# Performance work log

Hardware: AMD Instinct MI355X
Metric: run time of the kernel (lower is better)

## Reference

```python
import jax, jax.numpy as jnp
import numpy as np

N_DIM = 1024   # nodes (rows of s, rows of Kweight)
IN_DIM = 1024  # nodes / feature dim (cols of s, rows of Qweight, side of Gmat)
H_DIM = 64
B = 16


def setup_inputs() -> dict:
    key = jax.random.key(0)
    k1, k2, k3, k4 = jax.random.split(key, 4)
    s = jax.random.normal(k1, (N_DIM, B, IN_DIM), dtype=jnp.float32)
    Gmat = jax.random.uniform(k2, (IN_DIM, IN_DIM), dtype=jnp.float32)
    # torch init: rand * (4/d)**0.5 - (1/d)**0.5  => U[-(1/d)**0.5, (1/d)**0.5]... kept faithful
    Qweight = jax.random.uniform(k3, (IN_DIM, H_DIM), dtype=jnp.float32) * (4.0 / IN_DIM) ** 0.5 - (1.0 / IN_DIM) ** 0.5
    Kweight = jax.random.uniform(k4, (N_DIM, H_DIM), dtype=jnp.float32) * (4.0 / N_DIM) ** 0.5 - (1.0 / N_DIM) ** 0.5
    return {"s": s, "Gmat": Gmat, "Qweight": Qweight, "Kweight": Kweight}


def reference(s, Gmat, Qweight, Kweight):
    h_dim = Qweight.shape[1]
    inv_sqrt_h = 1.0 / jnp.sqrt(jnp.float32(h_dim))
    # q: einsum('ijk,km->ijm', s, Qw).permute(1,0,2) -> (B, n, h)
    q = jnp.einsum('nbi,ih->bnh', s, Qweight)
    # k: s.permute(1,2,0) einsum Kw then permute(0,2,1) -> (B, h, i)
    k = jnp.einsum('nbi,nh->bhi', s, Kweight)
    # squared (non-softmax) attention scores: (B, n, i)
    att = jnp.square(jnp.einsum('bnh,bhi->bni', q, k) * inv_sqrt_h + 1e-9)
    # adjacency aggregation: (B, n, i) @ (i, i)
    att = jnp.einsum('bni,ij->bnj', att, Gmat)
    # row-normalize and permute back to (n, B, i)
    s_t = jnp.sum(att, axis=2, keepdims=True) + 0.001
    return (att / s_t).transpose(1, 0, 2)
```

## Files before the change

### kernel.cpp

```cpp
#include <hip/hip_runtime.h>
#include <hip/hip_bf16.h>
#include <stdint.h>

typedef unsigned short u16;
typedef unsigned int   u32;

#define N_DIM  1024
#define IN_DIM 1024
#define H_DIM  64
#define BATCH  16

typedef __bf16 bf16x8 __attribute__((ext_vector_type(8)));
typedef float  f32x4  __attribute__((ext_vector_type(4)));

__device__ inline u16 f2bf(float f) {
    union { float f; u32 u; } v; v.f = f;
    u32 u = v.u;
    return (u16)((u + 0x7fffu + ((u >> 16) & 1u)) >> 16);
}
__device__ inline u32 pack2(float a, float b) {
    __hip_bfloat162 h = __float22bfloat162_rn(float2{a, b});
    union { __hip_bfloat162 h; u32 u; } cv; cv.h = h; return cv.u;
}

__device__ inline void gl_lds16(const u16* g, u16* l) {
    __builtin_amdgcn_global_load_lds(
        (const __attribute__((address_space(1))) u32*)g,
        (__attribute__((address_space(3))) u32*)l, 16, 0, 0);
}

__global__ void prep_w(const float* __restrict__ Q, const float* __restrict__ Kw,
                       u16* __restrict__ QT, u16* __restrict__ KwT) {
    int idx = blockIdx.x * 256 + threadIdx.x;
    const float* src = (idx < 65536) ? Q : Kw;
    u16* dst = (idx < 65536) ? QT : KwT;
    int i = idx & 65535;
    int h = i >> 10;
    int n = i & 1023;
    dst[h * 1024 + n] = f2bf(src[n * 64 + h]);
}

__global__ void prep_g(const float* __restrict__ G, u16* __restrict__ Gbt,
                       float* __restrict__ Grsum) {
    __shared__ float tile[64][65];
    int i0 = blockIdx.y * 64, j0 = blockIdx.x * 64;
    int tx = threadIdx.x & 63, ty = threadIdx.x >> 6;
    for (int r = 0; r < 16; ++r) {
        int i = ty * 16 + r;
        tile[i][tx] = G[(size_t)(i0 + i) * 1024 + j0 + tx];
    }
    __syncthreads();
    for (int r = 0; r < 16; ++r) {
        int j = ty * 16 + r;
        Gbt[(size_t)(j0 + j) * 1024 + i0 + tx] = f2bf(tile[tx][j]);
    }
    if (ty == 0) {
        float sum = 0.f;
        for (int j = 0; j < 64; ++j) sum += tile[tx][j];
        atomicAdd(&Grsum[i0 + tx], sum);
    }
}

__global__ __launch_bounds__(512) void gemm_q(
        const float* __restrict__ s, const u16* __restrict__ QT,
        u16* __restrict__ qws) {
    int b = blockIdx.y;
    int n0 = blockIdx.x * 64;
    __shared__ __align__(16) float red[4096];
    int t = threadIdx.x, lane = t & 63, w = t >> 6, quad = lane >> 4, l15 = lane & 15;
    int wm = (w & 3) * 16;
    int kb = (w >> 2) * 512;
    const float* arow = s + (size_t)(n0 + wm + l15) * (BATCH * IN_DIM)
                          + (size_t)b * IN_DIM + kb + quad * 8;
    const u16* bbase = QT + (size_t)l15 * 1024 + kb + quad * 8;

    f32x4 acc[4] = {};
    float4 A0[2], A1[2];
    bf16x8 Bf[2][4];
    A0[0] = ((const float4*)arow)[0];
    A1[0] = ((const float4*)arow)[1];
#pragma unroll
    for (int ct = 0; ct < 4; ++ct)
        Bf[0][ct] = *(const bf16x8*)&bbase[ct * 16384];

#pragma unroll
    for (int st = 0; st < 16; ++st) {
        int cur = st & 1, nxt = cur ^ 1;
        if (st < 15) {
            const float4* ap = (const float4*)(arow + (size_t)(st + 1) * 32);
            A0[nxt] = ap[0];
            A1[nxt] = ap[1];
#pragma unroll
            for (int ct = 0; ct < 4; ++ct)
                Bf[nxt][ct] = *(const bf16x8*)&bbase[ct * 16384 + (st + 1) * 32];
        }
        float4 fa = A0[cur], fb = A1[cur];
        union { uint4 u; bf16x8 v; } cu;
        cu.u = (uint4){ pack2(fa.x, fa.y), pack2(fa.z, fa.w),
                        pack2(fb.x, fb.y), pack2(fb.z, fb.w) };
#pragma unroll
        for (int ct = 0; ct < 4; ++ct)
            acc[ct] = __builtin_amdgcn_mfma_f32_16x16x32_bf16(cu.v, Bf[cur][ct], acc[ct], 0, 0, 0);
    }

    if (w >= 4) {
        float* dst = red + ((w - 4) * 64 + lane) * 16;
#pragma unroll
        for (int ct = 0; ct < 4; ++ct) *(f32x4*)&dst[ct * 4] = acc[ct];
    }
    __syncthreads();
    if (w < 4) {
        const float* sp2 = red + (w * 64 + lane) * 16;
        u16* ob = qws + (size_t)b * 65536;
#pragma unroll
        for (int ct = 0; ct < 4; ++ct) {
            f32x4 o = *(const f32x4*)&sp2[ct * 4];
#pragma unroll
            for (int r = 0; r < 4; ++r) {
                int m = n0 + wm + quad * 4 + r;
                ob[(size_t)m * 64 + ct * 16 + l15] = f2bf(acc[ct][r] + o[r]);
            }
        }
    }
}

__global__ __launch_bounds__(512) void gemm_kt(
        const float* __restrict__ s, const u16* __restrict__ KwT,
        u16* __restrict__ ktws) {
    int b = blockIdx.y;
    int i0 = blockIdx.x * 64;
    __shared__ __align__(16) u16 As[2][2][64][34];
    int t = threadIdx.x, lane = t & 63, w = t >> 6, quad = lane >> 4, l15 = lane & 15;
    int half = w >> 2;
    int wm = (w & 3) * 16;
    int shalf = t >> 8, nr = (t & 255) >> 3, iofs = (t & 7) * 8;
    const float* sp = s + (size_t)(shalf * 512 + nr) * (BATCH * IN_DIM)
                        + (size_t)b * IN_DIM + i0 + iofs;
    const u16* bbase = KwT + (size_t)l15 * 1024 + half * 512 + quad * 8;

    f32x4 acc[4] = {};
    float4 P0[2], P1[2];
    bf16x8 Bf[2][4];
    P0[0] = ((const float4*)sp)[0];
    P1[0] = ((const float4*)sp)[1];
    {
        const float4* p = (const float4*)(sp + (size_t)32 * 16384);
        P0[1] = p[0]; P1[1] = p[1];
    }
#pragma unroll
    for (int ct = 0; ct < 4; ++ct)
        Bf[0][ct] = *(const bf16x8*)&bbase[ct * 16384];

#pragma unroll
    for (int c = 0; c < 16; ++c) {
        int buf = c & 1;
        float4 fa = P0[buf], fb = P1[buf];
        u16* wp = &As[shalf][buf][iofs][nr];
        wp[0]   = f2bf(fa.x);
        wp[34]  = f2bf(fa.y);
        wp[68]  = f2bf(fa.z);
        wp[102] = f2bf(fa.w);
        wp[136] = f2bf(fb.x);
        wp[170] = f2bf(fb.y);
        wp[204] = f2bf(fb.z);
        wp[238] = f2bf(fb.w);
        __syncthreads();
        if (c < 14) {
            const float4* p = (const float4*)(sp + (size_t)(c + 2) * 32 * 16384);
            P0[buf] = p[0]; P1[buf] = p[1];
        }
        if (c < 15) {
#pragma unroll
            for (int ct = 0; ct < 4; ++ct)
                Bf[(c + 1) & 1][ct] = *(const bf16x8*)&bbase[ct * 16384 + (c + 1) * 32];
        }
        const u32* ap = (const u32*)&As[half][buf][wm + l15][quad * 8];
        union { u32 u[4]; bf16x8 v; } au;
        au.u[0] = ap[0]; au.u[1] = ap[1]; au.u[2] = ap[2]; au.u[3] = ap[3];
#pragma unroll
        for (int ct = 0; ct < 4; ++ct)
            acc[ct] = __builtin_amdgcn_mfma_f32_16x16x32_bf16(au.v, Bf[buf][ct], acc[ct], 0, 0, 0);
    }

    __syncthreads();
    float* red = (float*)As;
    if (w >= 4) {
        float* dst = red + ((w - 4) * 64 + lane) * 16;
#pragma unroll
        for (int ct = 0; ct < 4; ++ct) *(f32x4*)&dst[ct * 4] = acc[ct];
    }
    __syncthreads();
    if (w < 4) {
        const float* sp2 = red + (w * 64 + lane) * 16;
        u16* ob = ktws + (size_t)b * 65536;
#pragma unroll
        for (int ct = 0; ct < 4; ++ct) {
            f32x4 o = *(const f32x4*)&sp2[ct * 4];
#pragma unroll
            for (int r = 0; r < 4; ++r) {
                int i = i0 + wm + quad * 4 + r;
                ob[(size_t)i * 64 + ct * 16 + l15] = f2bf(acc[ct][r] + o[r]);
            }
        }
    }
}

__global__ __launch_bounds__(256, 2) void gemm_fused(
        const u16* __restrict__ qws, const u16* __restrict__ ktws,
        const u16* __restrict__ Gbt, const float* __restrict__ Grsum,
        float* __restrict__ out) {
    int b = blockIdx.z;
    int n0 = blockIdx.x * 256, m0 = blockIdx.y * 128;
    const u16* qb = qws  + (size_t)b * 65536;
    const u16* kb = ktws + (size_t)b * 65536;
    __shared__ __align__(16) u16 As[128 * 40];
    __shared__ __align__(16) u16 Bs[2][256 * 32];
    __shared__ __align__(16) u16 ktc[32 * 72];
    __shared__ __align__(16) float Grs[1024];
    __shared__ float rs[128];
    int t = threadIdx.x, lane = t & 63, w = t >> 6, quad = lane >> 4, l15 = lane & 15;
    int ti = w & 1;
    int wm = (w >> 1) * 64;
    int wn = (w & 1) * 128;

    ((float4*)Grs)[t] = ((const float4*)Grsum)[t];
    if (t < 128) rs[t] = 0.f;

    bf16x8 qf[4][2];
    for (int j = 0; j < 4; ++j)
        for (int kick = 0; kick < 2; ++kick)
            qf[j][kick] = *(const bf16x8*)&qb[(size_t)(m0 + wm + j*16 + l15) * 64 + kick*32 + quad*8];

    int br = t >> 2, bc = (t & 3) * 8;
    for (int g4 = 0; g4 < 4; ++g4)
        gl_lds16(Gbt + (size_t)(n0 + br + g4*64) * 1024 + bc, &Bs[0][(br + g4*64) * 32 + bc]);
    int ir = t >> 3, ch = (t & 7) * 8;
    uint4 kreg = *(const uint4*)&kb[(size_t)ir * 64 + ch];

    f32x4 acc[4][8] = {};
    float partial[4] = {0.f, 0.f, 0.f, 0.f};

    for (int kk = 0; kk < 32; ++kk) {
        int buf = kk & 1;
        *(uint4*)&ktc[ir * 72 + ch] = kreg;
        __syncthreads();
        f32x4 sacc[4] = {};
        for (int kick = 0; kick < 2; ++kick) {
            bf16x8 ktf = *(const bf16x8*)&ktc[(ti*16 + l15) * 72 + kick*32 + quad*8];
            for (int j = 0; j < 4; ++j)
                sacc[j] = __builtin_amdgcn_mfma_f32_16x16x32_bf16(ktf, qf[j][kick], sacc[j], 0, 0, 0);
        }
        if (kk < 31)
            kreg = *(const uint4*)&kb[(size_t)((kk + 1) * 32 + ir) * 64 + ch];
        float4 g = *(const float4*)&Grs[kk * 32 + ti * 16 + quad * 4];
        for (int j = 0; j < 4; ++j) {
            float v0 = sacc[j][0] * 0.125f + 1e-9f; v0 *= v0;
            float v1 = sacc[j][1] * 0.125f + 1e-9f; v1 *= v1;
            float v2 = sacc[j][2] * 0.125f + 1e-9f; v2 *= v2;
            float v3 = sacc[j][3] * 0.125f + 1e-9f; v3 *= v3;
            partial[j] += v0 * g.x + v1 * g.y + v2 * g.z + v3 * g.w;
            uint2 pk = { pack2(v0, v1), pack2(v2, v3) };
            *(uint2*)&As[(wm + j*16 + l15) * 40 + ti*16 + quad*4] = pk;
        }
        __syncthreads();
        if (kk < 31) {
            for (int g4 = 0; g4 < 4; ++g4)
                gl_lds16(Gbt + (size_t)(n0 + br + g4*64) * 1024 + (kk+1)*32 + bc,
                         &Bs[buf^1][(br + g4*64) * 32 + bc]);
        }
        int kh = quad * 8;
        bf16x8 af[4];
        for (int i = 0; i < 4; ++i) af[i] = *(const bf16x8*)&As[(wm + i*16 + l15) * 40 + kh];
        for (int jh = 0; jh < 2; ++jh) {
            bf16x8 bfr[4];
            for (int j = 0; j < 4; ++j)
                bfr[j] = *(const bf16x8*)&Bs[buf][(wn + jh*64 + j*16 + l15) * 32 + kh];
            for (int i = 0; i < 4; ++i)
                for (int j = 0; j < 4; ++j)
                    acc[i][jh*4 + j] = __builtin_amdgcn_mfma_f32_16x16x32_bf16(af[i], bfr[j], acc[i][jh*4 + j], 0, 0, 0);
        }
    }

    for (int j = 0; j < 4; ++j) {
        partial[j] += __shfl_xor(partial[j], 16, 64);
        partial[j] += __shfl_xor(partial[j], 32, 64);
    }
    if (quad == 0)
        for (int j = 0; j < 4; ++j) atomicAdd(&rs[wm + j*16 + l15], partial[j]);
    __syncthreads();
    if (t < 128) rs[t] = 1.0f / (rs[t] + 0.001f);
    __syncthreads();

    for (int i = 0; i < 4; ++i) {
        float4 rv = *(const float4*)&rs[wm + i * 16 + quad * 4];
        float rva[4] = { rv.x, rv.y, rv.z, rv.w };
        for (int r = 0; r < 4; ++r) {
            int m = m0 + wm + i * 16 + quad * 4 + r;
            float* orow = out + (size_t)m * (BATCH * IN_DIM) + (size_t)b * IN_DIM + n0 + wn;
            for (int j = 0; j < 8; ++j)
                orow[j * 16 + l15] = acc[i][j][r] * rva[r];
        }
    }
}

extern "C" void kernel_launch(void* const* d_in, const int* in_sizes, int n_in,
                              void* d_out, int out_size, void* d_ws, size_t ws_size,
                              hipStream_t stream) {
    const float* s  = (const float*)d_in[0];
    const float* G  = (const float*)d_in[1];
    const float* Q  = (const float*)d_in[2];
    const float* Kw = (const float*)d_in[3];
    float* out = (float*)d_out;
    char* ws = (char*)d_ws;

    u16*   qws   = (u16*)(ws + (size_t)(32u << 20));
    u16*   ktws  = qws + (size_t)16 * 65536;
    u16*   Gbt   = (u16*)(ws + (size_t)(36u << 20));
    u16*   QT    = (u16*)(ws + (size_t)(38u << 20));
    u16*   KwT   = (u16*)(ws + (size_t)(38u << 20) + (128u << 10));
    float* Grsum = (float*)(ws + (size_t)(38u << 20) + (256u << 10));

    hipMemsetAsync(Grsum, 0, 1024 * sizeof(float), stream);
    prep_w<<<512, 256, 0, stream>>>(Q, Kw, QT, KwT);
    prep_g<<<dim3(16, 16), 256, 0, stream>>>(G, Gbt, Grsum);
    gemm_q<<<dim3(16, 16), 512, 0, stream>>>(s, QT, qws);
    gemm_kt<<<dim3(16, 16), 512, 0, stream>>>(s, KwT, ktws);
    gemm_fused<<<dim3(4, 8, 16), 256, 0, stream>>>(qws, ktws, Gbt, Grsum, out);
}
```

Baseline: 204.9 us.

## Merge prep and projection kernels, swizzle G tile LDS, deepen q prefetch

```diff
diff --git a/kernel.cpp b/kernel.cpp
--- a/kernel.cpp
+++ b/kernel.cpp
@@ -29,21 +29,24 @@
         (__attribute__((address_space(3))) u32*)l, 16, 0, 0);
 }
 
-__global__ void prep_w(const float* __restrict__ Q, const float* __restrict__ Kw,
-                       u16* __restrict__ QT, u16* __restrict__ KwT) {
-    int idx = blockIdx.x * 256 + threadIdx.x;
-    const float* src = (idx < 65536) ? Q : Kw;
-    u16* dst = (idx < 65536) ? QT : KwT;
-    int i = idx & 65535;
-    int h = i >> 10;
-    int n = i & 1023;
-    dst[h * 1024 + n] = f2bf(src[n * 64 + h]);
-}
-
-__global__ void prep_g(const float* __restrict__ G, u16* __restrict__ Gbt,
-                       float* __restrict__ Grsum) {
+__global__ __launch_bounds__(256) void prep(
+        const float* __restrict__ G, const float* __restrict__ Q,
+        const float* __restrict__ Kw, u16* __restrict__ Gbt,
+        float* __restrict__ Grp, u16* __restrict__ QT, u16* __restrict__ KwT) {
+    int bid = blockIdx.x;
+    if (bid >= 256) {
+        int idx = (bid - 256) * 256 + threadIdx.x;
+        const float* src = (idx < 65536) ? Q : Kw;
+        u16* dst = (idx < 65536) ? QT : KwT;
+        int i = idx & 65535;
+        int h = i >> 10;
+        int n = i & 1023;
+        dst[h * 1024 + n] = f2bf(src[n * 64 + h]);
+        return;
+    }
     __shared__ float tile[64][65];
-    int i0 = blockIdx.y * 64, j0 = blockIdx.x * 64;
+    int jt = bid & 15, it = bid >> 4;
+    int i0 = it * 64, j0 = jt * 64;
     int tx = threadIdx.x & 63, ty = threadIdx.x >> 6;
     for (int r = 0; r < 16; ++r) {
         int i = ty * 16 + r;
@@ -57,80 +60,89 @@
     if (ty == 0) {
         float sum = 0.f;
         for (int j = 0; j < 64; ++j) sum += tile[tx][j];
-        atomicAdd(&Grsum[i0 + tx], sum);
-    }
-}
-
-__global__ __launch_bounds__(512) void gemm_q(
+        Grp[jt * 1024 + i0 + tx] = sum;
+    }
+}
+
+__global__ __launch_bounds__(512, 4) void qkt(
         const float* __restrict__ s, const u16* __restrict__ QT,
-        u16* __restrict__ qws) {
+        const u16* __restrict__ KwT, const float* __restrict__ Grp,
+        u16* __restrict__ qws, u16* __restrict__ ktws, float* __restrict__ Grsum) {
     int b = blockIdx.y;
-    int n0 = blockIdx.x * 64;
-    __shared__ __align__(16) float red[4096];
     int t = threadIdx.x, lane = t & 63, w = t >> 6, quad = lane >> 4, l15 = lane & 15;
-    int wm = (w & 3) * 16;
-    int kb = (w >> 2) * 512;
-    const float* arow = s + (size_t)(n0 + wm + l15) * (BATCH * IN_DIM)
-                          + (size_t)b * IN_DIM + kb + quad * 8;
-    const u16* bbase = QT + (size_t)l15 * 1024 + kb + quad * 8;
-
-    f32x4 acc[4] = {};
-    float4 A0[2], A1[2];
-    bf16x8 Bf[2][4];
-    A0[0] = ((const float4*)arow)[0];
-    A1[0] = ((const float4*)arow)[1];
-#pragma unroll
-    for (int ct = 0; ct < 4; ++ct)
-        Bf[0][ct] = *(const bf16x8*)&bbase[ct * 16384];
-
-#pragma unroll
-    for (int st = 0; st < 16; ++st) {
-        int cur = st & 1, nxt = cur ^ 1;
-        if (st < 15) {
-            const float4* ap = (const float4*)(arow + (size_t)(st + 1) * 32);
-            A0[nxt] = ap[0];
-            A1[nxt] = ap[1];
+    __shared__ __align__(16) u16 sh[2][2][64][34];
+    float* red = (float*)sh;
+
+    if (blockIdx.z == 0) {
+        if (blockIdx.y == 0 && t < 64) {
+            int i = blockIdx.x * 64 + t;
+            float g = 0.f;
+            for (int jt = 0; jt < 16; ++jt) g += Grp[jt * 1024 + i];
+            Grsum[i] = g;
+        }
+        int n0 = blockIdx.x * 64;
+        int wm = (w & 3) * 16;
+        int kb = (w >> 2) * 512;
+        const float* arow = s + (size_t)(n0 + wm + l15) * (BATCH * IN_DIM)
+                              + (size_t)b * IN_DIM + kb + quad * 8;
+        const u16* bbase = QT + (size_t)l15 * 1024 + kb + quad * 8;
+
+        f32x4 acc[4] = {};
+        float4 A0[3], A1[3];
+        bf16x8 Bf[2][4];
+        A0[0] = ((const float4*)arow)[0];
+        A1[0] = ((const float4*)arow)[1];
+        A0[1] = ((const float4*)(arow + 32))[0];
+        A1[1] = ((const float4*)(arow + 32))[1];
+#pragma unroll
+        for (int ct = 0; ct < 4; ++ct)
+            Bf[0][ct] = *(const bf16x8*)&bbase[ct * 16384];
+
+#pragma unroll
+        for (int st = 0; st < 16; ++st) {
+            int cur = st % 3, cb = st & 1;
+            if (st < 14) {
+                const float4* ap = (const float4*)(arow + (size_t)(st + 2) * 32);
+                A0[(st + 2) % 3] = ap[0];
+                A1[(st + 2) % 3] = ap[1];
+            }
+            if (st < 15) {
+#pragma unroll
+                for (int ct = 0; ct < 4; ++ct)
+                    Bf[cb ^ 1][ct] = *(const bf16x8*)&bbase[ct * 16384 + (st + 1) * 32];
+            }
+            float4 fa = A0[cur], fb = A1[cur];
+            union { uint4 u; bf16x8 v; } cu;
+            cu.u = (uint4){ pack2(fa.x, fa.y), pack2(fa.z, fa.w),
+                            pack2(fb.x, fb.y), pack2(fb.z, fb.w) };
 #pragma unroll
             for (int ct = 0; ct < 4; ++ct)
-                Bf[nxt][ct] = *(const bf16x8*)&bbase[ct * 16384 + (st + 1) * 32];
-        }
-        float4 fa = A0[cur], fb = A1[cur];
-        union { uint4 u; bf16x8 v; } cu;
-        cu.u = (uint4){ pack2(fa.x, fa.y), pack2(fa.z, fa.w),
-                        pack2(fb.x, fb.y), pack2(fb.z, fb.w) };
-#pragma unroll
-        for (int ct = 0; ct < 4; ++ct)
-            acc[ct] = __builtin_amdgcn_mfma_f32_16x16x32_bf16(cu.v, Bf[cur][ct], acc[ct], 0, 0, 0);
-    }
-
-    if (w >= 4) {
-        float* dst = red + ((w - 4) * 64 + lane) * 16;
-#pragma unroll
-        for (int ct = 0; ct < 4; ++ct) *(f32x4*)&dst[ct * 4] = acc[ct];
-    }
-    __syncthreads();
-    if (w < 4) {
-        const float* sp2 = red + (w * 64 + lane) * 16;
-        u16* ob = qws + (size_t)b * 65536;
-#pragma unroll
-        for (int ct = 0; ct < 4; ++ct) {
-            f32x4 o = *(const f32x4*)&sp2[ct * 4];
-#pragma unroll
-            for (int r = 0; r < 4; ++r) {
-                int m = n0 + wm + quad * 4 + r;
-                ob[(size_t)m * 64 + ct * 16 + l15] = f2bf(acc[ct][r] + o[r]);
+                acc[ct] = __builtin_amdgcn_mfma_f32_16x16x32_bf16(cu.v, Bf[cb][ct], acc[ct], 0, 0, 0);
+        }
+
+        if (w >= 4) {
+            float* dst = red + ((w - 4) * 64 + lane) * 16;
+#pragma unroll
+            for (int ct = 0; ct < 4; ++ct) *(f32x4*)&dst[ct * 4] = acc[ct];
+        }
+        __syncthreads();
+        if (w < 4) {
+            const float* sp2 = red + (w * 64 + lane) * 16;
+            u16* ob = qws + (size_t)b * 65536;
+#pragma unroll
+            for (int ct = 0; ct < 4; ++ct) {
+                f32x4 o = *(const f32x4*)&sp2[ct * 4];
+#pragma unroll
+                for (int r = 0; r < 4; ++r) {
+                    int m = n0 + wm + quad * 4 + r;
+                    ob[(size_t)m * 64 + ct * 16 + l15] = f2bf(acc[ct][r] + o[r]);
+                }
             }
         }
-    }
-}
-
-__global__ __launch_bounds__(512) void gemm_kt(
-        const float* __restrict__ s, const u16* __restrict__ KwT,
-        u16* __restrict__ ktws) {
-    int b = blockIdx.y;
+        return;
+    }
+
     int i0 = blockIdx.x * 64;
-    __shared__ __align__(16) u16 As[2][2][64][34];
-    int t = threadIdx.x, lane = t & 63, w = t >> 6, quad = lane >> 4, l15 = lane & 15;
     int half = w >> 2;
     int wm = (w & 3) * 16;
     int shalf = t >> 8, nr = (t & 255) >> 3, iofs = (t & 7) * 8;
@@ -155,7 +167,7 @@
     for (int c = 0; c < 16; ++c) {
         int buf = c & 1;
         float4 fa = P0[buf], fb = P1[buf];
-        u16* wp = &As[shalf][buf][iofs][nr];
+        u16* wp = &sh[shalf][buf][iofs][nr];
         wp[0]   = f2bf(fa.x);
         wp[34]  = f2bf(fa.y);
         wp[68]  = f2bf(fa.z);
@@ -174,7 +186,7 @@
             for (int ct = 0; ct < 4; ++ct)
                 Bf[(c + 1) & 1][ct] = *(const bf16x8*)&bbase[ct * 16384 + (c + 1) * 32];
         }
-        const u32* ap = (const u32*)&As[half][buf][wm + l15][quad * 8];
+        const u32* ap = (const u32*)&sh[half][buf][wm + l15][quad * 8];
         union { u32 u[4]; bf16x8 v; } au;
         au.u[0] = ap[0]; au.u[1] = ap[1]; au.u[2] = ap[2]; au.u[3] = ap[3];
 #pragma unroll
@@ -183,7 +195,6 @@
     }
 
     __syncthreads();
-    float* red = (float*)As;
     if (w >= 4) {
         float* dst = red + ((w - 4) * 64 + lane) * 16;
 #pragma unroll
@@ -231,11 +242,12 @@
         for (int kick = 0; kick < 2; ++kick)
             qf[j][kick] = *(const bf16x8*)&qb[(size_t)(m0 + wm + j*16 + l15) * 64 + kick*32 + quad*8];
 
-    int br = t >> 2, bc = (t & 3) * 8;
+    int br = t >> 2, bc = ((t & 3) ^ (br & 3)) * 8;
     for (int g4 = 0; g4 < 4; ++g4)
-        gl_lds16(Gbt + (size_t)(n0 + br + g4*64) * 1024 + bc, &Bs[0][(br + g4*64) * 32 + bc]);
+        gl_lds16(Gbt + (size_t)(n0 + br + g4*64) * 1024 + bc, &Bs[0][(br + g4*64) * 32 + (t & 3) * 8]);
     int ir = t >> 3, ch = (t & 7) * 8;
     uint4 kreg = *(const uint4*)&kb[(size_t)ir * 64 + ch];
+    int khs = (quad ^ (l15 & 3)) * 8;
 
     f32x4 acc[4][8] = {};
     float partial[4] = {0.f, 0.f, 0.f, 0.f};
@@ -266,7 +278,7 @@
         if (kk < 31) {
             for (int g4 = 0; g4 < 4; ++g4)
                 gl_lds16(Gbt + (size_t)(n0 + br + g4*64) * 1024 + (kk+1)*32 + bc,
-                         &Bs[buf^1][(br + g4*64) * 32 + bc]);
+                         &Bs[buf^1][(br + g4*64) * 32 + (t & 3) * 8]);
         }
         int kh = quad * 8;
         bf16x8 af[4];
@@ -274,7 +286,7 @@
         for (int jh = 0; jh < 2; ++jh) {
             bf16x8 bfr[4];
             for (int j = 0; j < 4; ++j)
-                bfr[j] = *(const bf16x8*)&Bs[buf][(wn + jh*64 + j*16 + l15) * 32 + kh];
+                bfr[j] = *(const bf16x8*)&Bs[buf][(wn + jh*64 + j*16 + l15) * 32 + khs];
             for (int i = 0; i < 4; ++i)
                 for (int j = 0; j < 4; ++j)
                     acc[i][jh*4 + j] = __builtin_amdgcn_mfma_f32_16x16x32_bf16(af[i], bfr[j], acc[i][jh*4 + j], 0, 0, 0);
@@ -313,17 +325,15 @@
     float* out = (float*)d_out;
     char* ws = (char*)d_ws;
 
-    u16*   qws   = (u16*)(ws + (size_t)(32u << 20));
-    u16*   ktws  = qws + (size_t)16 * 65536;
-    u16*   Gbt   = (u16*)(ws + (size_t)(36u << 20));
-    u16*   QT    = (u16*)(ws + (size_t)(38u << 20));
-    u16*   KwT   = (u16*)(ws + (size_t)(38u << 20) + (128u << 10));
-    float* Grsum = (float*)(ws + (size_t)(38u << 20) + (256u << 10));
-
-    hipMemsetAsync(Grsum, 0, 1024 * sizeof(float), stream);
-    prep_w<<<512, 256, 0, stream>>>(Q, Kw, QT, KwT);
-    prep_g<<<dim3(16, 16), 256, 0, stream>>>(G, Gbt, Grsum);
-    gemm_q<<<dim3(16, 16), 512, 0, stream>>>(s, QT, qws);
-    gemm_kt<<<dim3(16, 16), 512, 0, stream>>>(s, KwT, ktws);
+    u16*   qws   = (u16*)(ws);
+    u16*   ktws  = (u16*)(ws + (size_t)(2u << 20));
+    u16*   Gbt   = (u16*)(ws + (size_t)(4u << 20));
+    u16*   QT    = (u16*)(ws + (size_t)(6u << 20));
+    u16*   KwT   = (u16*)(ws + (size_t)(6u << 20) + (128u << 10));
+    float* Grsum = (float*)(ws + (size_t)(6u << 20) + (256u << 10));
+    float* Grp   = (float*)(ws + (size_t)(6u << 20) + (260u << 10));
+
+    prep<<<768, 256, 0, stream>>>(G, Q, Kw, Gbt, Grp, QT, KwT);
+    qkt<<<dim3(16, 16, 2), 512, 0, stream>>>(s, QT, KwT, Grp, qws, ktws, Grsum);
     gemm_fused<<<dim3(4, 8, 16), 256, 0, stream>>>(qws, ktws, Gbt, Grsum, out);
 }
```

Measured after the change: 197.5 us. 1.04x faster.
